# Kernel optimization log

Measured on AMD Instinct MI355X. Metric: run time of the kernel, lower is better.

Reference implementation:

```python
import jax, jax.numpy as jnp
import numpy as np

LATENT = 64

def _linear(x, W, b):
    return x @ W.T + b

def setup_inputs() -> dict:
    key = jax.random.key(0)
    ks = jax.random.split(key, 16)
    B, D, H, L = 16384, 784, 1024, LATENT
    def u(k, shape, fan_in):
        bound = 1.0 / np.sqrt(fan_in)
        return jax.random.uniform(k, shape, jnp.float32, -bound, bound)
    inp = {
        "x": jax.random.uniform(ks[0], (B, D), jnp.float32),
        "epsilon": jax.random.normal(ks[1], (B, L), jnp.float32),
        "W_ih": u(ks[2], (H, D), D), "b_ih": u(ks[3], (H,), D),
        "W_m":  u(ks[4], (L, H), H), "b_m":  u(ks[5], (L,), H),
        "W_lv": u(ks[6], (L, H), H), "b_lv": u(ks[7], (L,), H),
        "W_ap": u(ks[8], (L, H), H), "b_ap": u(ks[9], (L,), H),
        "W_lh": u(ks[10], (H, L), L), "b_lh": u(ks[11], (H,), L),
        "W_ho": u(ks[12], (D, H), H), "b_ho": u(ks[13], (D,), H),
    }
    return inp

def reference(x, epsilon, W_ih, b_ih, W_m, b_m, W_lv, b_lv, W_ap, b_ap, W_lh, b_lh, W_ho, b_ho):
    # ----- encode -----
    hidden = jnp.tanh(_linear(x, W_ih, b_ih))            # [B,H]
    mean   = _linear(hidden, W_m, b_m)                   # [B,L]
    logvar = jnp.clip(_linear(hidden, W_lv, b_lv), -4.5, 0.0)  # Hardtanh(-4.5,0)
    approx = _linear(hidden, W_ap, b_ap)                 # [B,L]
    # ----- reparameterize (rank-1 Gaussian) -----
    # inv_cov = diag(exp(logvar)) + approx approx^T   per sample
    B, L = mean.shape
    eye = jnp.eye(L, dtype=mean.dtype)
    inv_cov = jnp.exp(logvar)[:, :, None] * eye + approx[:, :, None] * approx[:, None, :]  # [B,L,L]
    cov = jnp.linalg.inv(inv_cov)                        # batched 64x64 inverse
    # torch.potrf default returns UPPER Cholesky U with U^T U = cov -> U = chol(cov).T
    Sigma = jnp.swapaxes(jnp.linalg.cholesky(cov), -1, -2)  # [B,L,L] upper
    z = mean + jnp.einsum('bij,bj->bi', Sigma, epsilon)  # [B,L]
    # ----- decode -----
    h2 = jnp.tanh(_linear(z, W_lh, b_lh))
    x_mean = jax.nn.sigmoid(_linear(h2, W_ho, b_ho))     # [B,784]
    return (x_mean, z, mean, logvar, approx)
```

## Files before the change

### kernel.cpp

```cpp
#include <hip/hip_runtime.h>
#include <hip/hip_bf16.h>
#include <math.h>

typedef __attribute__((ext_vector_type(8))) short short8;
typedef __attribute__((ext_vector_type(4))) float f32x4;
typedef __attribute__((ext_vector_type(4))) unsigned short us4;

#define GLOBAL_AS __attribute__((address_space(1)))
#define LDS_AS __attribute__((address_space(3)))

__device__ inline void g2l16(const void* g, void* l) {
    __builtin_amdgcn_global_load_lds((const GLOBAL_AS void*)g, (LDS_AS void*)l, 16, 0, 0);
}

__device__ inline unsigned short f2bf(float f) {
    unsigned int u = __float_as_uint(f);
    return (unsigned short)((u + 0x7fffu + ((u >> 16) & 1u)) >> 16);
}

template <int EPI>
__global__ __launch_bounds__(512, 4) void mgemmB(
    const __hip_bfloat16* __restrict__ A,
    const __hip_bfloat16* __restrict__ W,
    const float* __restrict__ bias,
    void* __restrict__ outp,
    int lda, int ldb, int nT, int ldc, int Nreal)
{
    __shared__ __align__(16) __hip_bfloat16 sh[2][12288];

    const int tid  = threadIdx.x;
    const int wave = tid >> 6;
    const int lane = tid & 63;
    const int rBase = blockIdx.x * 256;
    const int cBase = blockIdx.y * 128;

    const __hip_bfloat16* Ab = A + (size_t)rBase * lda;
    const __hip_bfloat16* Wb = W + (size_t)cBase * ldb;

    const int wr = (wave >> 1) * 64;
    const int wc = (wave & 1) * 64;
    const int h  = lane >> 4;
    const int r0 = lane & 15;
    const int swz = h ^ ((r0 >> 1) & 3);

    f32x4 acc[4][4];
#pragma unroll
    for (int m = 0; m < 4; ++m)
#pragma unroll
        for (int n = 0; n < 4; ++n) acc[m][n] = (f32x4){0.f, 0.f, 0.f, 0.f};

    auto stage = [&](int bb, int t) {
        const int k0 = t * 32;
#pragma unroll
        for (int r = 0; r < 2; ++r) {
            int s2  = r * 512 + tid;
            int row = s2 >> 2;
            int cg  = (s2 & 3) ^ ((row >> 1) & 3);
            g2l16(Ab + (size_t)row * lda + k0 + cg * 8, &sh[bb][s2 * 8]);
        }
        {
            int s2  = tid;
            int row = s2 >> 2;
            int cg  = (s2 & 3) ^ ((row >> 1) & 3);
            g2l16(Wb + (size_t)row * ldb + k0 + cg * 8, &sh[bb][8192 + s2 * 8]);
        }
    };

    auto compute = [&](int bb) {
        const __hip_bfloat16* base = &sh[bb][0];
        short8 a_[4], b_[4];
#pragma unroll
        for (int m = 0; m < 4; ++m) {
            int R = wr + m * 16 + r0;
            a_[m] = *(const short8*)(base + (R * 4 + swz) * 8);
        }
#pragma unroll
        for (int n = 0; n < 4; ++n) {
            int R = wc + n * 16 + r0;
            b_[n] = *(const short8*)(base + 8192 + (R * 4 + swz) * 8);
        }
        __builtin_amdgcn_s_setprio(1);
#pragma unroll
        for (int m = 0; m < 4; ++m)
#pragma unroll
            for (int n = 0; n < 4; ++n)
                acc[m][n] = __builtin_amdgcn_mfma_f32_16x16x32_bf16(a_[m], b_[n], acc[m][n], 0, 0, 0);
        __builtin_amdgcn_s_setprio(0);
    };

    stage(0, 0);
    stage(1, 1);
    for (int t = 0; t < nT; ++t) {
        const int cur = t & 1;
        if (t + 1 < nT) asm volatile("s_waitcnt vmcnt(3)" ::: "memory");
        else            asm volatile("s_waitcnt vmcnt(0)" ::: "memory");
        __builtin_amdgcn_s_barrier();
        compute(cur);
        __builtin_amdgcn_s_barrier();
        if (t + 2 < nT) stage(cur, t + 2);
    }

    const int rq = lane >> 4;
    const int c0 = lane & 15;
#pragma unroll
    for (int m = 0; m < 4; ++m) {
#pragma unroll
        for (int n = 0; n < 4; ++n) {
            f32x4 v = acc[m][n];
            const int gc = cBase + wc + n * 16 + c0;
            const float bv = bias[gc];
#pragma unroll
            for (int j = 0; j < 4; ++j) {
                const int gr = rBase + wr + m * 16 + rq * 4 + j;
                float val = v[j] + bv;
                if (EPI == 1) {
                    ((__hip_bfloat16*)outp)[(size_t)gr * ldc + gc] = __float2bfloat16(tanhf(val));
                } else {
                    if (gc < Nreal)
                        ((float*)outp)[(size_t)gr * Nreal + gc] = 1.f / (1.f + expf(-val));
                }
            }
        }
    }
}

template <int EPI>
__global__ __launch_bounds__(256) void mgemm(
    const __hip_bfloat16* __restrict__ A,
    const __hip_bfloat16* __restrict__ W,
    const float* __restrict__ bias,
    void* __restrict__ outp,
    int lda, int ldb, int nT, int ldc, int Nreal)
{
    __shared__ __align__(16) __hip_bfloat16 sh[2][8192];

    const int tid  = threadIdx.x;
    const int wave = tid >> 6;
    const int lane = tid & 63;
    const int rBase = blockIdx.x * 128;
    const int cBase = blockIdx.y * 128;

    const __hip_bfloat16* Ab = A + (size_t)rBase * lda;
    const __hip_bfloat16* Wb = W + (size_t)cBase * ldb;

    const int wr = (wave >> 1) * 64;
    const int wc = (wave & 1) * 64;
    const int h  = lane >> 4;
    const int r0 = lane & 15;
    const int swz = h ^ ((r0 >> 1) & 3);

    f32x4 acc[4][4];
#pragma unroll
    for (int m = 0; m < 4; ++m)
#pragma unroll
        for (int n = 0; n < 4; ++n) acc[m][n] = (f32x4){0.f, 0.f, 0.f, 0.f};

    auto stage = [&](int bb, int k0) {
#pragma unroll
        for (int r = 0; r < 2; ++r) {
            int s2  = r * 256 + tid;
            int row = s2 >> 2;
            int cg  = (s2 & 3) ^ ((row >> 1) & 3);
            g2l16(Ab + (size_t)row * lda + k0 + cg * 8, &sh[bb][s2 * 8]);
            g2l16(Wb + (size_t)row * ldb + k0 + cg * 8, &sh[bb][4096 + s2 * 8]);
        }
    };

    auto compute = [&](int bb) {
        const __hip_bfloat16* base = &sh[bb][0];
        short8 a_[4], b_[4];
#pragma unroll
        for (int m = 0; m < 4; ++m) {
            int R = wr + m * 16 + r0;
            a_[m] = *(const short8*)(base + (R * 4 + swz) * 8);
        }
#pragma unroll
        for (int n = 0; n < 4; ++n) {
            int R = wc + n * 16 + r0;
            b_[n] = *(const short8*)(base + 4096 + (R * 4 + swz) * 8);
        }
#pragma unroll
        for (int m = 0; m < 4; ++m)
#pragma unroll
            for (int n = 0; n < 4; ++n)
                acc[m][n] = __builtin_amdgcn_mfma_f32_16x16x32_bf16(a_[m], b_[n], acc[m][n], 0, 0, 0);
    };

    stage(0, 0);
    __syncthreads();
    int cur = 0;
    for (int t = 0; t < nT; ++t) {
        if (t + 1 < nT) stage(cur ^ 1, (t + 1) * 32);
        compute(cur);
        __syncthreads();
        cur ^= 1;
    }

    const int rq = lane >> 4;
    const int c0 = lane & 15;
#pragma unroll
    for (int m = 0; m < 4; ++m) {
#pragma unroll
        for (int n = 0; n < 4; ++n) {
            f32x4 v = acc[m][n];
            const int gc = cBase + wc + n * 16 + c0;
            const float bv = bias[gc];
#pragma unroll
            for (int j = 0; j < 4; ++j) {
                const int gr = rBase + wr + m * 16 + rq * 4 + j;
                float val = v[j] + bv;
                if (EPI == 0) {
                    const int sel = gc >> 6, cc = gc & 63;
                    if (sel < 3) {
                        if (sel == 1) val = fminf(fmaxf(val, -4.5f), 0.f);
                        ((float*)outp)[(size_t)sel * (16384u * 64u) + (size_t)gr * 64 + cc] = val;
                    }
                } else if (EPI == 1) {
                    ((__hip_bfloat16*)outp)[(size_t)gr * ldc + gc] = __float2bfloat16(tanhf(val));
                }
            }
        }
    }
}

__global__ void cvt_pad4(const float* __restrict__ src, unsigned short* __restrict__ dst,
                         int scols, int dcols, long total4)
{
    long i = (long)blockIdx.x * 256 + threadIdx.x;
    if (i >= total4) return;
    long e = i * 4;
    long row = e / dcols;
    int  c = (int)(e - row * dcols);
    us4 o = (us4){0, 0, 0, 0};
    if (c < scols) {
        float4 v = *(const float4*)(src + row * (long)scols + c);
        o.x = f2bf(v.x); o.y = f2bf(v.y); o.z = f2bf(v.z); o.w = f2bf(v.w);
    }
    *(us4*)(dst + e) = o;
}

__global__ void cvt_rows4(const float* __restrict__ src, unsigned short* __restrict__ dst,
                          int srows, long total4)
{
    long i = (long)blockIdx.x * 256 + threadIdx.x;
    if (i >= total4) return;
    long e = i * 4;
    int r = (int)(e >> 10), c = (int)(e & 1023);
    us4 o = (us4){0, 0, 0, 0};
    if (r < srows) {
        float4 v = *(const float4*)(src + (size_t)r * 1024 + c);
        o.x = f2bf(v.x); o.y = f2bf(v.y); o.z = f2bf(v.z); o.w = f2bf(v.w);
    }
    *(us4*)(dst + e) = o;
}

__global__ void pack_heads(const float* __restrict__ Wm, const float* __restrict__ Wlv,
                           const float* __restrict__ Wap, __hip_bfloat16* __restrict__ dst)
{
    int i = blockIdx.x * 256 + threadIdx.x;
    int r = i >> 10, c = i & 1023;
    float v = 0.f;
    if (r < 64)       v = Wm[(size_t)r * 1024 + c];
    else if (r < 128) v = Wlv[(size_t)(r - 64) * 1024 + c];
    else if (r < 192) v = Wap[(size_t)(r - 128) * 1024 + c];
    dst[i] = __float2bfloat16(v);
}

__global__ void pack_bias3(const float* bm, const float* blv, const float* bap, float* dst)
{
    int i = threadIdx.x;
    float v = 0.f;
    if (i < 64)       v = bm[i];
    else if (i < 128) v = blv[i - 64];
    else if (i < 192) v = bap[i - 128];
    dst[i] = v;
}

__global__ void pad_vec(const float* src, float* dst, int n, int total)
{
    int i = blockIdx.x * 256 + threadIdx.x;
    if (i >= total) return;
    dst[i] = (i < n) ? src[i] : 0.f;
}

__global__ __launch_bounds__(256) void reparam_kernel(
    const float* __restrict__ mean, const float* __restrict__ logvar,
    const float* __restrict__ approx, const float* __restrict__ eps,
    float* __restrict__ z, __hip_bfloat16* __restrict__ zb, int B)
{
    const int gid  = blockIdx.x * 256 + threadIdx.x;
    const int row  = gid >> 6;
    const int lane = threadIdx.x & 63;
    if (row >= B) return;

    const size_t idx = (size_t)row * 64 + lane;
    const float m  = mean[idx];
    const float lv = logvar[idx];
    const float a  = approx[idx];
    const float ep = eps[idx];

    const float s  = expf(-lv);
    const float x1 = a * a * s;
    const float x2 = s * a * ep;

    float R = x1, S = x2;
#pragma unroll
    for (int off = 1; off < 64; off <<= 1) {
        float r2 = __shfl_down(R, off, 64);
        float s2 = __shfl_down(S, off, 64);
        if (lane + off < 64) { R += r2; S += s2; }
    }
    const float Rexc  = R - x1;
    const float Sexc  = S - x2;
    const float inv1R = 1.f / (1.f + R);
    const float dL    = sqrtf(s * (1.f + Rexc) * inv1R);
    const float bj    = -s * a * inv1R / dL;

    const float zv = m + dL * ep + bj * Sexc;
    z[idx]  = zv;
    zb[idx] = __float2bfloat16(zv);
}

extern "C" void kernel_launch(void* const* d_in, const int* in_sizes, int n_in,
                              void* d_out, int out_size, void* d_ws, size_t ws_size,
                              hipStream_t stream)
{
    const float* x    = (const float*)d_in[0];
    const float* eps  = (const float*)d_in[1];
    const float* W_ih = (const float*)d_in[2];
    const float* b_ih = (const float*)d_in[3];
    const float* W_m  = (const float*)d_in[4];
    const float* b_m  = (const float*)d_in[5];
    const float* W_lv = (const float*)d_in[6];
    const float* b_lv = (const float*)d_in[7];
    const float* W_ap = (const float*)d_in[8];
    const float* b_ap = (const float*)d_in[9];
    const float* W_lh = (const float*)d_in[10];
    const float* b_lh = (const float*)d_in[11];
    const float* W_ho = (const float*)d_in[12];
    const float* b_ho = (const float*)d_in[13];

    const int B = 16384;

    float* out    = (float*)d_out;
    float* x_mean = out;
    float* z      = out + (size_t)B * 784;
    float* mean   = z + (size_t)B * 64;
    float* logvar = mean + (size_t)B * 64;
    float* approx = logvar + (size_t)B * 64;

    char* ws = (char*)d_ws;
    __hip_bfloat16* hb    = (__hip_bfloat16*)(ws + 0);
    __hip_bfloat16* xb    = (__hip_bfloat16*)(ws + 33554432);
    __hip_bfloat16* wihb  = (__hip_bfloat16*)(ws + 60817408);
    __hip_bfloat16* whead = (__hip_bfloat16*)(ws + 62521344);
    __hip_bfloat16* wlhb  = (__hip_bfloat16*)(ws + 63045632);
    __hip_bfloat16* whob  = (__hip_bfloat16*)(ws + 63176704);
    float*          bhead = (float*)(ws + 65273856);
    float*          bho   = (float*)(ws + 65274880);
    __hip_bfloat16* h2b   = hb;
    __hip_bfloat16* zb    = xb;

    long g;
    g = (long)B * 832 / 4;
    cvt_pad4<<<dim3((g + 255) / 256), dim3(256), 0, stream>>>(x, (unsigned short*)xb, 784, 832, g);
    g = 1024L * 832 / 4;
    cvt_pad4<<<dim3((g + 255) / 256), dim3(256), 0, stream>>>(W_ih, (unsigned short*)wihb, 784, 832, g);
    pack_heads<<<dim3(1024), dim3(256), 0, stream>>>(W_m, W_lv, W_ap, whead);
    pack_bias3<<<dim3(1), dim3(256), 0, stream>>>(b_m, b_lv, b_ap, bhead);
    g = 1024L * 64 / 4;
    cvt_pad4<<<dim3((g + 255) / 256), dim3(256), 0, stream>>>(W_lh, (unsigned short*)wlhb, 64, 64, g);
    g = 896L * 1024 / 4;
    cvt_rows4<<<dim3((g + 255) / 256), dim3(256), 0, stream>>>(W_ho, (unsigned short*)whob, 784, g);
    pad_vec<<<dim3(4), dim3(256), 0, stream>>>(b_ho, bho, 784, 896);

    mgemmB<1><<<dim3(64, 8), dim3(512), 0, stream>>>(xb, wihb, b_ih, hb, 832, 832, 26, 1024, 1024);

    mgemm<0><<<dim3(128, 2), dim3(256), 0, stream>>>(hb, whead, bhead, mean, 1024, 1024, 32, 0, 192);

    reparam_kernel<<<dim3((B * 64) / 256), dim3(256), 0, stream>>>(mean, logvar, approx, eps, z, zb, B);

    mgemm<1><<<dim3(128, 8), dim3(256), 0, stream>>>(zb, wlhb, b_lh, h2b, 64, 64, 2, 1024, 1024);

    mgemmB<2><<<dim3(64, 7), dim3(512), 0, stream>>>(h2b, whob, bho, x_mean, 1024, 1024, 32, 784, 784);
}
```

Before: 160.5 us.

## Fuse prep kernels, deepen mgemm prefetch pipeline, raise mgemmB occupancy hint

Seven small conversion and packing launches are merged into two kernels, prep1 and prep2, with prep2 moved after the first GEMM and its outputs placed in reused workspace. The small GEMM now prefetches two stages ahead, using explicit vmcnt waits and raw barriers instead of __syncthreads, and raises wave priority around the MFMA block. The launch bounds of mgemmB go from 4 to 6, which may force register spills. Together these aim to cut launch overhead and expose more load/compute overlap.

```diff
diff --git a/kernel.cpp b/kernel.cpp
--- a/kernel.cpp
+++ b/kernel.cpp
@@ -19,7 +19,7 @@
 }
 
 template <int EPI>
-__global__ __launch_bounds__(512, 4) void mgemmB(
+__global__ __launch_bounds__(512, 6) void mgemmB(
     const __hip_bfloat16* __restrict__ A,
     const __hip_bfloat16* __restrict__ W,
     const float* __restrict__ bias,
@@ -125,7 +125,7 @@
 }
 
 template <int EPI>
-__global__ __launch_bounds__(256) void mgemm(
+__global__ __launch_bounds__(256, 4) void mgemmC(
     const __hip_bfloat16* __restrict__ A,
     const __hip_bfloat16* __restrict__ W,
     const float* __restrict__ bias,
@@ -155,7 +155,8 @@
 #pragma unroll
         for (int n = 0; n < 4; ++n) acc[m][n] = (f32x4){0.f, 0.f, 0.f, 0.f};
 
-    auto stage = [&](int bb, int k0) {
+    auto stage = [&](int bb, int t) {
+        const int k0 = t * 32;
 #pragma unroll
         for (int r = 0; r < 2; ++r) {
             int s2  = r * 256 + tid;
@@ -179,21 +180,25 @@
             int R = wc + n * 16 + r0;
             b_[n] = *(const short8*)(base + 4096 + (R * 4 + swz) * 8);
         }
+        __builtin_amdgcn_s_setprio(1);
 #pragma unroll
         for (int m = 0; m < 4; ++m)
 #pragma unroll
             for (int n = 0; n < 4; ++n)
                 acc[m][n] = __builtin_amdgcn_mfma_f32_16x16x32_bf16(a_[m], b_[n], acc[m][n], 0, 0, 0);
+        __builtin_amdgcn_s_setprio(0);
     };
 
     stage(0, 0);
-    __syncthreads();
-    int cur = 0;
+    stage(1, 1);
     for (int t = 0; t < nT; ++t) {
-        if (t + 1 < nT) stage(cur ^ 1, (t + 1) * 32);
+        const int cur = t & 1;
+        if (t + 1 < nT) asm volatile("s_waitcnt vmcnt(4)" ::: "memory");
+        else            asm volatile("s_waitcnt vmcnt(0)" ::: "memory");
+        __builtin_amdgcn_s_barrier();
         compute(cur);
-        __syncthreads();
-        cur ^= 1;
+        __builtin_amdgcn_s_barrier();
+        if (t + 2 < nT) stage(cur, t + 2);
     }
 
     const int rq = lane >> 4;
@@ -223,64 +228,82 @@
     }
 }
 
-__global__ void cvt_pad4(const float* __restrict__ src, unsigned short* __restrict__ dst,
-                         int scols, int dcols, long total4)
-{
-    long i = (long)blockIdx.x * 256 + threadIdx.x;
-    if (i >= total4) return;
-    long e = i * 4;
-    long row = e / dcols;
-    int  c = (int)(e - row * dcols);
-    us4 o = (us4){0, 0, 0, 0};
-    if (c < scols) {
-        float4 v = *(const float4*)(src + row * (long)scols + c);
+__global__ void prep1(const float* __restrict__ x, const float* __restrict__ Wih,
+                      const float* __restrict__ Wm, const float* __restrict__ Wlv,
+                      const float* __restrict__ Wap, const float* __restrict__ bm,
+                      const float* __restrict__ blv, const float* __restrict__ bap,
+                      const float* __restrict__ bho_src,
+                      unsigned short* __restrict__ xw,
+                      unsigned short* __restrict__ whead,
+                      float* __restrict__ bhead, float* __restrict__ bho)
+{
+    const long SEG0 = 17408L * 208, SEG1 = SEG0 + 65536, SEG2 = SEG1 + 64, SEG3 = SEG2 + 256;
+    long u = (long)blockIdx.x * 256 + threadIdx.x;
+    if (u < SEG0) {
+        long r = u / 208;
+        int  c = (int)(u - r * 208) * 4;
+        us4 o = (us4){0, 0, 0, 0};
+        if (c < 784) {
+            const float* src = (r < 16384) ? (x + r * 784) : (Wih + (r - 16384) * 784);
+            float4 v = *(const float4*)(src + c);
+            o.x = f2bf(v.x); o.y = f2bf(v.y); o.z = f2bf(v.z); o.w = f2bf(v.w);
+        }
+        *(us4*)(xw + r * 832 + c) = o;
+    } else if (u < SEG1) {
+        long t = u - SEG0;
+        int r = (int)(t >> 8), c = (int)(t & 255) * 4;
+        us4 o = (us4){0, 0, 0, 0};
+        const float* src = nullptr;
+        if (r < 64)       src = Wm + (size_t)r * 1024;
+        else if (r < 128) src = Wlv + (size_t)(r - 64) * 1024;
+        else if (r < 192) src = Wap + (size_t)(r - 128) * 1024;
+        if (src) {
+            float4 v = *(const float4*)(src + c);
+            o.x = f2bf(v.x); o.y = f2bf(v.y); o.z = f2bf(v.z); o.w = f2bf(v.w);
+        }
+        *(us4*)(whead + (size_t)r * 1024 + c) = o;
+    } else if (u < SEG2) {
+        int base = (int)(u - SEG1) * 4;
+#pragma unroll
+        for (int k = 0; k < 4; ++k) {
+            int p = base + k;
+            float v = 0.f;
+            if (p < 64)       v = bm[p];
+            else if (p < 128) v = blv[p - 64];
+            else if (p < 192) v = bap[p - 128];
+            bhead[p] = v;
+        }
+    } else if (u < SEG3) {
+        int base = (int)(u - SEG2) * 4;
+#pragma unroll
+        for (int k = 0; k < 4; ++k) {
+            int p = base + k;
+            bho[p] = (p < 784) ? bho_src[p] : 0.f;
+        }
+    }
+}
+
+__global__ void prep2(const float* __restrict__ Who, const float* __restrict__ Wlh,
+                      unsigned short* __restrict__ whob, unsigned short* __restrict__ wlhb)
+{
+    const long SEG0 = 262144, SEG1 = SEG0 + 16384;
+    long u = (long)blockIdx.x * 256 + threadIdx.x;
+    if (u < SEG0) {
+        int r = (int)(u >> 8), c = (int)(u & 255) * 4;
+        us4 o = (us4){0, 0, 0, 0};
+        if (r < 784) {
+            float4 v = *(const float4*)(Who + (size_t)r * 1024 + c);
+            o.x = f2bf(v.x); o.y = f2bf(v.y); o.z = f2bf(v.z); o.w = f2bf(v.w);
+        }
+        *(us4*)(whob + (size_t)r * 1024 + c) = o;
+    } else if (u < SEG1) {
+        long t = u - SEG0;
+        int r = (int)(t >> 4), c = (int)(t & 15) * 4;
+        float4 v = *(const float4*)(Wlh + (size_t)r * 64 + c);
+        us4 o;
         o.x = f2bf(v.x); o.y = f2bf(v.y); o.z = f2bf(v.z); o.w = f2bf(v.w);
-    }
-    *(us4*)(dst + e) = o;
-}
-
-__global__ void cvt_rows4(const float* __restrict__ src, unsigned short* __restrict__ dst,
-                          int srows, long total4)
-{
-    long i = (long)blockIdx.x * 256 + threadIdx.x;
-    if (i >= total4) return;
-    long e = i * 4;
-    int r = (int)(e >> 10), c = (int)(e & 1023);
-    us4 o = (us4){0, 0, 0, 0};
-    if (r < srows) {
-        float4 v = *(const float4*)(src + (size_t)r * 1024 + c);
-        o.x = f2bf(v.x); o.y = f2bf(v.y); o.z = f2bf(v.z); o.w = f2bf(v.w);
-    }
-    *(us4*)(dst + e) = o;
-}
-
-__global__ void pack_heads(const float* __restrict__ Wm, const float* __restrict__ Wlv,
-                           const float* __restrict__ Wap, __hip_bfloat16* __restrict__ dst)
-{
-    int i = blockIdx.x * 256 + threadIdx.x;
-    int r = i >> 10, c = i & 1023;
-    float v = 0.f;
-    if (r < 64)       v = Wm[(size_t)r * 1024 + c];
-    else if (r < 128) v = Wlv[(size_t)(r - 64) * 1024 + c];
-    else if (r < 192) v = Wap[(size_t)(r - 128) * 1024 + c];
-    dst[i] = __float2bfloat16(v);
-}
-
-__global__ void pack_bias3(const float* bm, const float* blv, const float* bap, float* dst)
-{
-    int i = threadIdx.x;
-    float v = 0.f;
-    if (i < 64)       v = bm[i];
-    else if (i < 128) v = blv[i - 64];
-    else if (i < 192) v = bap[i - 128];
-    dst[i] = v;
-}
-
-__global__ void pad_vec(const float* src, float* dst, int n, int total)
-{
-    int i = blockIdx.x * 256 + threadIdx.x;
-    if (i >= total) return;
-    dst[i] = (i < n) ? src[i] : 0.f;
+        *(us4*)(wlhb + (size_t)r * 64 + c) = o;
+    }
 }
 
 __global__ __launch_bounds__(256) void reparam_kernel(
@@ -354,33 +377,30 @@
     __hip_bfloat16* xb    = (__hip_bfloat16*)(ws + 33554432);
     __hip_bfloat16* wihb  = (__hip_bfloat16*)(ws + 60817408);
     __hip_bfloat16* whead = (__hip_bfloat16*)(ws + 62521344);
-    __hip_bfloat16* wlhb  = (__hip_bfloat16*)(ws + 63045632);
-    __hip_bfloat16* whob  = (__hip_bfloat16*)(ws + 63176704);
     float*          bhead = (float*)(ws + 65273856);
     float*          bho   = (float*)(ws + 65274880);
+    __hip_bfloat16* zb    = (__hip_bfloat16*)(ws + 33554432);
+    __hip_bfloat16* whob  = (__hip_bfloat16*)(ws + 37748736);
+    __hip_bfloat16* wlhb  = (__hip_bfloat16*)(ws + 39845888);
     __hip_bfloat16* h2b   = hb;
-    __hip_bfloat16* zb    = xb;
-
-    long g;
-    g = (long)B * 832 / 4;
-    cvt_pad4<<<dim3((g + 255) / 256), dim3(256), 0, stream>>>(x, (unsigned short*)xb, 784, 832, g);
-    g = 1024L * 832 / 4;
-    cvt_pad4<<<dim3((g + 255) / 256), dim3(256), 0, stream>>>(W_ih, (unsigned short*)wihb, 784, 832, g);
-    pack_heads<<<dim3(1024), dim3(256), 0, stream>>>(W_m, W_lv, W_ap, whead);
-    pack_bias3<<<dim3(1), dim3(256), 0, stream>>>(b_m, b_lv, b_ap, bhead);
-    g = 1024L * 64 / 4;
-    cvt_pad4<<<dim3((g + 255) / 256), dim3(256), 0, stream>>>(W_lh, (unsigned short*)wlhb, 64, 64, g);
-    g = 896L * 1024 / 4;
-    cvt_rows4<<<dim3((g + 255) / 256), dim3(256), 0, stream>>>(W_ho, (unsigned short*)whob, 784, g);
-    pad_vec<<<dim3(4), dim3(256), 0, stream>>>(b_ho, bho, 784, 896);
+
+    {
+        long total = 17408L * 208 + 65536 + 64 + 256;
+        prep1<<<dim3((total + 255) / 256), dim3(256), 0, stream>>>(
+            x, W_ih, W_m, W_lv, W_ap, b_m, b_lv, b_ap, b_ho,
+            (unsigned short*)xb, (unsigned short*)whead, bhead, bho);
+    }
 
     mgemmB<1><<<dim3(64, 8), dim3(512), 0, stream>>>(xb, wihb, b_ih, hb, 832, 832, 26, 1024, 1024);
 
-    mgemm<0><<<dim3(128, 2), dim3(256), 0, stream>>>(hb, whead, bhead, mean, 1024, 1024, 32, 0, 192);
+    prep2<<<dim3((262144 + 16384 + 255) / 256), dim3(256), 0, stream>>>(
+        W_ho, W_lh, (unsigned short*)whob, (unsigned short*)wlhb);
+
+    mgemmC<0><<<dim3(128, 2), dim3(256), 0, stream>>>(hb, whead, bhead, mean, 1024, 1024, 32, 0, 192);
 
     reparam_kernel<<<dim3((B * 64) / 256), dim3(256), 0, stream>>>(mean, logvar, approx, eps, z, zb, B);
 
-    mgemm<1><<<dim3(128, 8), dim3(256), 0, stream>>>(zb, wlhb, b_lh, h2b, 64, 64, 2, 1024, 1024);
+    mgemmC<1><<<dim3(128, 8), dim3(256), 0, stream>>>(zb, wlhb, b_lh, h2b, 64, 64, 2, 1024, 1024);
 
     mgemmB<2><<<dim3(64, 7), dim3(512), 0, stream>>>(h2b, whob, bho, x_mean, 1024, 1024, 32, 784, 784);
 }
```

New measurement: 498.5 us. 3.11x slower.
